# Kernel optimization log

Measured on AMD Instinct MI355X. Metric: run time of the kernel, lower is better.

The kernel has to match this reference:

```python
import jax, jax.numpy as jnp
import numpy as np

B, T, DIN, DOUT = 32, 3136, 192, 384
H, QS, WS = 6, 4, 16            # heads, q_stride, window_size (post-pool)
HD = DOUT // H                   # head_dim = 64
INNER = QS * WS                  # tokens per mask unit before pooling = 64
NW = T // INNER                  # num_windows = 49
MLP_HID = 4 * DOUT
EPS = 1e-5


def layer_norm(x, w, b):
    mu = x.mean(-1, keepdims=True)
    var = ((x - mu) ** 2).mean(-1, keepdims=True)
    return (x - mu) * jax.lax.rsqrt(var + EPS) * w + b


def setup_inputs() -> dict:
    key = jax.random.key(0)
    ks = jax.random.split(key, 16)
    rn = lambda k, shp, fan: jax.random.normal(k, shp, jnp.float32) * (fan ** -0.5)
    return {
        "embeddings": jax.random.normal(ks[0], (B, T, DIN), jnp.float32),
        "norm1_w": jnp.ones((DIN,), jnp.float32),
        "norm1_b": jnp.zeros((DIN,), jnp.float32),
        "w_qkv": rn(ks[1], (3 * DOUT, DIN), DIN),
        "b_qkv": jnp.zeros((3 * DOUT,), jnp.float32),
        "w_attn_proj": rn(ks[2], (DOUT, DOUT), DOUT),
        "b_attn_proj": jnp.zeros((DOUT,), jnp.float32),
        "w_res_proj": rn(ks[3], (DOUT, DIN), DIN),
        "b_res_proj": jnp.zeros((DOUT,), jnp.float32),
        "norm2_w": jnp.ones((DOUT,), jnp.float32),
        "norm2_b": jnp.zeros((DOUT,), jnp.float32),
        "w_fc1": rn(ks[4], (MLP_HID, DOUT), DOUT),
        "b_fc1": jnp.zeros((MLP_HID,), jnp.float32),
        "w_fc2": rn(ks[5], (DOUT, MLP_HID), MLP_HID),
        "b_fc2": jnp.zeros((DOUT,), jnp.float32),
    }


def _block(embeddings, norm1_w, norm1_b, w_qkv, b_qkv, w_attn_proj, b_attn_proj,
           w_res_proj, b_res_proj, norm2_w, norm2_b, w_fc1, b_fc1, w_fc2, b_fc2):
    x = layer_norm(embeddings, norm1_w, norm1_b)                 # [B,T,DIN]

    # residual path: project then do_pool (max over q_stride groups)
    res = x @ w_res_proj.T + b_res_proj                          # [B,T,DOUT]
    res = res.reshape(B, QS, T // QS, DOUT).max(axis=1)          # [B,T/QS,DOUT]

    # mask-unit attention
    qkv = x @ w_qkv.T + b_qkv                                    # [B,T,3*DOUT]
    qkv = qkv.reshape(B, INNER, NW, 3, H, HD)
    qkv = jnp.transpose(qkv, (3, 0, 4, 2, 1, 5))                 # [3,B,H,NW,INNER,HD]
    q, k, v = qkv[0], qkv[1], qkv[2]
    q = q.reshape(B, H, NW, QS, WS, HD).max(axis=3)              # q-pool -> [B,H,NW,WS,HD]
    scale = HD ** -0.5
    attn = jax.nn.softmax(jnp.einsum("bhwqd,bhwkd->bhwqk", q * scale, k), axis=-1)
    out = jnp.einsum("bhwqk,bhwkd->bhwqd", attn, v)              # [B,H,NW,WS,HD]
    out = jnp.transpose(out, (0, 3, 2, 1, 4)).reshape(B, WS * NW, DOUT)
    out = out @ w_attn_proj.T + b_attn_proj

    emb = res + out
    h = layer_norm(emb, norm2_w, norm2_b)
    h = jax.nn.gelu(h @ w_fc1.T + b_fc1, approximate=False)
    emb = emb + (h @ w_fc2.T + b_fc2)
    return emb, attn


def reference(embeddings, norm1_w, norm1_b, w_qkv, b_qkv, w_attn_proj, b_attn_proj,
              w_res_proj, b_res_proj, norm2_w, norm2_b, w_fc1, b_fc1, w_fc2, b_fc2):
    return _block(embeddings, norm1_w, norm1_b, w_qkv, b_qkv, w_attn_proj, b_attn_proj,
                  w_res_proj, b_res_proj, norm2_w, norm2_b, w_fc1, b_fc1, w_fc2, b_fc2)
```

## Files before the change

### kernel.cpp

```cpp
#include <hip/hip_runtime.h>
#include <stdint.h>

typedef __bf16 bf16_t;
typedef __attribute__((ext_vector_type(8))) __bf16 bf16x8;
typedef __attribute__((ext_vector_type(4))) __bf16 bf16x4;
typedef __attribute__((ext_vector_type(4))) float f32x4;

#define NB_ 32
#define NT_ 3136
#define DIN_ 192
#define DOUT_ 384
#define NH_ 6
#define HD_ 64
#define NW_ 49
#define WSZ_ 16
#define TP_ 784
#define MLP_ 1536

__device__ __forceinline__ f32x4 mfma16(bf16x8 a, bf16x8 b, f32x4 c) {
  return __builtin_amdgcn_mfma_f32_16x16x32_bf16(a, b, c, 0, 0, 0);
}

__device__ __forceinline__ void gload_lds16(const bf16_t* g, bf16_t* l) {
  __builtin_amdgcn_global_load_lds(
      (const __attribute__((address_space(1))) void*)((const void*)g),
      (__attribute__((address_space(3))) void*)l, 16, 0, 0);
}

__device__ __forceinline__ float gelu_tanh(float v) {
  const float t2 = 1.5957691216f * (v + 0.044715f * v * v * v);
  return v * (1.f - 1.f / (1.f + __expf(t2)));
}

__global__ void cvt_kernel(const float* __restrict__ s0, const float* __restrict__ s1,
                           const float* __restrict__ s2, const float* __restrict__ s3,
                           const float* __restrict__ s4, bf16_t* __restrict__ d0,
                           bf16_t* __restrict__ d1, bf16_t* __restrict__ d2,
                           bf16_t* __restrict__ d3, bf16_t* __restrict__ d4) {
  const int b = blockIdx.x;
  const float* s; bf16_t* d; long off;
  if (b < 108)      { s = s0; d = d0; off = (long)b * 2048; }
  else if (b < 144) { s = s1; d = d1; off = (long)(b - 108) * 2048; }
  else if (b < 216) { s = s2; d = d2; off = (long)(b - 144) * 2048; }
  else if (b < 504) { s = s3; d = d3; off = (long)(b - 216) * 2048; }
  else              { s = s4; d = d4; off = (long)(b - 504) * 2048; }
  off += (long)threadIdx.x * 8;
  const float4 a = *(const float4*)(s + off);
  const float4 c = *(const float4*)(s + off + 4);
  bf16x8 o;
  o[0] = (bf16_t)a.x; o[1] = (bf16_t)a.y; o[2] = (bf16_t)a.z; o[3] = (bf16_t)a.w;
  o[4] = (bf16_t)c.x; o[5] = (bf16_t)c.y; o[6] = (bf16_t)c.z; o[7] = (bf16_t)c.w;
  *(bf16x8*)(d + off) = o;
}

template <int D>
__global__ void ln_f32_kernel(const float* __restrict__ in, const float* __restrict__ w,
                              const float* __restrict__ bvec, bf16_t* __restrict__ out) {
  const int row = blockIdx.x * 4 + (threadIdx.x >> 6);
  const int lane = threadIdx.x & 63;
  constexpr int PER = D / 64;
  const float* x = in + (long)row * D;
  float v[PER];
  float s = 0.f;
#pragma unroll
  for (int i = 0; i < PER; i++) { v[i] = x[lane * PER + i]; s += v[i]; }
#pragma unroll
  for (int off = 1; off < 64; off <<= 1) s += __shfl_xor(s, off);
  const float mu = s * (1.f / D);
  float s2 = 0.f;
#pragma unroll
  for (int i = 0; i < PER; i++) { const float d = v[i] - mu; s2 += d * d; }
#pragma unroll
  for (int off = 1; off < 64; off <<= 1) s2 += __shfl_xor(s2, off);
  const float rstd = rsqrtf(s2 * (1.f / D) + 1e-5f);
  bf16_t* o = out + (long)row * D;
#pragma unroll
  for (int i = 0; i < PER; i++) {
    const int c = lane * PER + i;
    o[c] = (bf16_t)((v[i] - mu) * rstd * w[c] + bvec[c]);
  }
}

template <int D>
__global__ void ln_bf16_kernel(const bf16_t* __restrict__ in, const float* __restrict__ w,
                               const float* __restrict__ bvec, bf16_t* __restrict__ out) {
  const int row = blockIdx.x * 4 + (threadIdx.x >> 6);
  const int lane = threadIdx.x & 63;
  constexpr int PER = D / 64;
  const bf16_t* x = in + (long)row * D;
  float v[PER];
  float s = 0.f;
#pragma unroll
  for (int i = 0; i < PER; i++) { v[i] = (float)x[lane * PER + i]; s += v[i]; }
#pragma unroll
  for (int off = 1; off < 64; off <<= 1) s += __shfl_xor(s, off);
  const float mu = s * (1.f / D);
  float s2 = 0.f;
#pragma unroll
  for (int i = 0; i < PER; i++) { const float d = v[i] - mu; s2 += d * d; }
#pragma unroll
  for (int off = 1; off < 64; off <<= 1) s2 += __shfl_xor(s2, off);
  const float rstd = rsqrtf(s2 * (1.f / D) + 1e-5f);
  bf16_t* o = out + (long)row * D;
#pragma unroll
  for (int i = 0; i < PER; i++) {
    const int c = lane * PER + i;
    o[c] = (bf16_t)((v[i] - mu) * rstd * w[c] + bvec[c]);
  }
}

template <int ACT, int POOL>
__global__ __launch_bounds__(512, 4) void gemm8(
    const bf16_t* __restrict__ A, const bf16_t* __restrict__ W,
    const float* __restrict__ bias, bf16_t* __restrict__ C,
    int M, int N, int K) {
  __shared__ __align__(16) char AsB[256 * 128];
  __shared__ __align__(16) char WsB[128 * 128];

  const int nwg = gridDim.x;
  const int q = nwg >> 3, rm = nwg & 7;
  const int xcd = blockIdx.x & 7, idx = blockIdx.x >> 3;
  const int wg = (xcd < rm ? xcd * (q + 1) : rm * (q + 1) + (xcd - rm) * q) + idx;

  const int nbn = N >> 7;
  const int bmi = wg / nbn;
  const int bni = wg - bmi * nbn;
  const int m0 = bmi << 8, n0 = bni << 7;
  const int tid = threadIdx.x;
  const int lane = tid & 63;
  const int wid = tid >> 6;
  const int wr = (wid >> 1) * 64, wc = (wid & 1) * 64;
  const int l15 = lane & 15;
  const int lkb = (lane >> 4) << 4;
  const int srow = tid >> 3;
  const int scolsw = ((tid & 7) << 3) ^ ((srow & 7) << 3);
  const int swzr = (l15 & 7) << 4;

  f32x4 acc[4][4];
  const f32x4 zero = {0.f, 0.f, 0.f, 0.f};
#pragma unroll
  for (int i = 0; i < 4; i++)
#pragma unroll
    for (int j = 0; j < 4; j++) acc[i][j] = zero;

  long arow[4];
#pragma unroll
  for (int p = 0; p < 4; p++) {
    const int m = m0 + p * 64 + srow;
    if constexpr (POOL) {
      const int b = m / NT_;
      const int mm = m - b * NT_;
      arow[p] = (long)b * NT_ + (mm & 3) * TP_ + (mm >> 2);
    } else {
      arow[p] = m;
    }
  }
  long wrow[2];
#pragma unroll
  for (int p = 0; p < 2; p++) wrow[p] = (long)(n0 + p * 64 + srow);

  for (int k0 = 0; k0 < K; k0 += 64) {
    __syncthreads();
#pragma unroll
    for (int p = 0; p < 4; p++)
      gload_lds16(A + arow[p] * K + k0 + scolsw, (bf16_t*)(AsB + p * 8192 + tid * 16));
#pragma unroll
    for (int p = 0; p < 2; p++)
      gload_lds16(W + wrow[p] * K + k0 + scolsw, (bf16_t*)(WsB + p * 8192 + tid * 16));
    __syncthreads();
#pragma unroll
    for (int kk = 0; kk < 2; kk++) {
      bf16x8 af[4], wf[4];
#pragma unroll
      for (int i = 0; i < 4; i++)
        af[i] = *(const bf16x8*)(AsB + (wr + i * 16 + l15) * 128 + ((kk * 64 + lkb) ^ swzr));
#pragma unroll
      for (int j = 0; j < 4; j++)
        wf[j] = *(const bf16x8*)(WsB + (wc + j * 16 + l15) * 128 + ((kk * 64 + lkb) ^ swzr));
#pragma unroll
      for (int i = 0; i < 4; i++)
#pragma unroll
        for (int j = 0; j < 4; j++) {
          if constexpr (POOL) acc[i][j] = mfma16(af[i], wf[j], acc[i][j]);
          else                acc[i][j] = mfma16(wf[j], af[i], acc[i][j]);
        }
    }
  }

  const int rg = (lane >> 4) * 4;
  if constexpr (POOL) {
#pragma unroll
    for (int j = 0; j < 4; j++) {
      const int gn = n0 + wc + j * 16 + l15;
      const float bv = bias[gn];
#pragma unroll
      for (int i = 0; i < 4; i++) {
        const float v = fmaxf(fmaxf(acc[i][j][0], acc[i][j][1]),
                              fmaxf(acc[i][j][2], acc[i][j][3])) + bv;
        const long pm = (long)((m0 + wr + i * 16 + rg) >> 2);
        C[pm * N + gn] = (bf16_t)v;
      }
    }
  } else {
    __syncthreads();
    char* scr = AsB + wid * 4096;
#pragma unroll
    for (int i = 0; i < 4; i++) {
#pragma unroll
      for (int j = 0; j < 4; j++)
        *(f32x4*)(scr + l15 * 256 + ((((j * 16 + rg) << 2)) ^ ((l15 & 7) << 4))) = acc[i][j];
#pragma unroll
      for (int k = 0; k < 4; k++) {
        const int rl = k * 4 + (lane >> 4);
        const int cb = (lane & 15) << 4;
        const f32x4 v = *(const f32x4*)(scr + rl * 256 + (cb ^ ((rl & 7) << 4)));
        const long gm = m0 + wr + i * 16 + rl;
        const int gn = n0 + wc + ((lane & 15) << 2);
        const float4 bv = *(const float4*)(bias + gn);
        float vv[4] = {v[0] + bv.x, v[1] + bv.y, v[2] + bv.z, v[3] + bv.w};
        if constexpr (ACT == 1) {
#pragma unroll
          for (int r = 0; r < 4; r++) vv[r] = gelu_tanh(vv[r]);
        }
        bf16x4 o;
#pragma unroll
        for (int r = 0; r < 4; r++) o[r] = (bf16_t)vv[r];
        *(bf16x4*)(C + gm * N + gn) = o;
      }
    }
  }
}

template <int HASRES, int OF32, int RF32>
__global__ __launch_bounds__(256) void gemm_t(
    const bf16_t* __restrict__ A, const bf16_t* __restrict__ W,
    const float* __restrict__ bias, const void* __restrict__ resv,
    void* __restrict__ Cv, int M, int N, int K) {
  constexpr int BM = 64;
  constexpr int PA = BM / 32;
  constexpr int ABYTES = BM * 128;
  constexpr int BUFSZ = ABYTES + 128 * 128;
  __shared__ __align__(16) char LDSB[2 * BUFSZ];

  const int nwg = gridDim.x;
  const int q = nwg >> 3, rm = nwg & 7;
  const int xcd = blockIdx.x & 7, idx = blockIdx.x >> 3;
  const int wg = (xcd < rm ? xcd * (q + 1) : rm * (q + 1) + (xcd - rm) * q) + idx;

  const int nbn = N >> 7;
  const int bmi = wg / nbn;
  const int bni = wg - bmi * nbn;
  const int m0 = bmi * BM, n0 = bni << 7;
  const int tid = threadIdx.x;
  const int lane = tid & 63;
  const int wid = tid >> 6;
  const int wr = (wid >> 1) * 32, wc = (wid & 1) * 64;
  const int l15 = lane & 15;
  const int lkb = (lane >> 4) << 4;
  const int srow = tid >> 3;
  const int scolsw = ((tid & 7) << 3) ^ ((srow & 7) << 3);
  const int swzr = (l15 & 7) << 4;

  f32x4 acc[PA][4];
  const f32x4 zero = {0.f, 0.f, 0.f, 0.f};
#pragma unroll
  for (int i = 0; i < PA; i++)
#pragma unroll
    for (int j = 0; j < 4; j++) acc[i][j] = zero;

  long arow[PA];
#pragma unroll
  for (int p = 0; p < PA; p++) arow[p] = m0 + srow + p * 32;
  long wrow[4];
#pragma unroll
  for (int p = 0; p < 4; p++) wrow[p] = (long)(n0 + srow + p * 32);

  auto stage = [&](int buf, int k0) {
    char* base = LDSB + buf * BUFSZ;
#pragma unroll
    for (int p = 0; p < PA; p++)
      gload_lds16(A + arow[p] * K + k0 + scolsw, (bf16_t*)(base + p * 4096 + tid * 16));
#pragma unroll
    for (int p = 0; p < 4; p++)
      gload_lds16(W + wrow[p] * K + k0 + scolsw,
                  (bf16_t*)(base + ABYTES + p * 4096 + tid * 16));
  };

  const int nt = K >> 6;
  stage(0, 0);
  int cur = 0;
  for (int t = 0; t < nt; t++) {
    __syncthreads();
    if (t + 1 < nt) stage(cur ^ 1, (t + 1) << 6);
    const char* base = LDSB + cur * BUFSZ;
#pragma unroll
    for (int kk = 0; kk < 2; kk++) {
      bf16x8 af[PA], wf[4];
#pragma unroll
      for (int i = 0; i < PA; i++)
        af[i] = *(const bf16x8*)(base + (wr + i * 16 + l15) * 128 + ((kk * 64 + lkb) ^ swzr));
#pragma unroll
      for (int j = 0; j < 4; j++)
        wf[j] = *(const bf16x8*)(base + ABYTES + (wc + j * 16 + l15) * 128 +
                                 ((kk * 64 + lkb) ^ swzr));
#pragma unroll
      for (int i = 0; i < PA; i++)
#pragma unroll
        for (int j = 0; j < 4; j++) acc[i][j] = mfma16(wf[j], af[i], acc[i][j]);
    }
    cur ^= 1;
  }

  __syncthreads();
  char* scr = LDSB + wid * 8192;
  const int rg = (lane >> 4) * 4;
#pragma unroll
  for (int i = 0; i < PA; i++) {
    const int ml = i * 16 + l15;
#pragma unroll
    for (int j = 0; j < 4; j++)
      *(f32x4*)(scr + ml * 256 + ((((j * 16 + rg) << 2)) ^ ((ml & 7) << 4))) = acc[i][j];
  }
#pragma unroll
  for (int k = 0; k < 8; k++) {
    const int rl = k * 4 + (lane >> 4);
    const int cb = (lane & 15) << 4;
    const f32x4 v = *(const f32x4*)(scr + rl * 256 + (cb ^ ((rl & 7) << 4)));
    const long gm = m0 + wr + rl;
    const int gn = n0 + wc + ((lane & 15) << 2);
    const float4 bv = *(const float4*)(bias + gn);
    float vv[4] = {v[0] + bv.x, v[1] + bv.y, v[2] + bv.z, v[3] + bv.w};
    if constexpr (HASRES) {
      if constexpr (RF32) {
        const float4 rv = *(const float4*)((const float*)resv + gm * N + gn);
        vv[0] += rv.x; vv[1] += rv.y; vv[2] += rv.z; vv[3] += rv.w;
      } else {
        const bf16x4 rv = *(const bf16x4*)((const bf16_t*)resv + gm * N + gn);
#pragma unroll
        for (int r = 0; r < 4; r++) vv[r] += (float)rv[r];
      }
    }
    if constexpr (OF32) {
      float4 o = {vv[0], vv[1], vv[2], vv[3]};
      *(float4*)((float*)Cv + gm * N + gn) = o;
    } else {
      bf16x4 o;
#pragma unroll
      for (int r = 0; r < 4; r++) o[r] = (bf16_t)vv[r];
      *(bf16x4*)((bf16_t*)Cv + gm * N + gn) = o;
    }
  }
}

__global__ __launch_bounds__(384) void qkv_attn_kernel(
    const bf16_t* __restrict__ x, const bf16_t* __restrict__ Wqkv,
    const float* __restrict__ bq, float* __restrict__ prob,
    bf16_t* __restrict__ obuf) {
  __shared__ __align__(16) char As[64 * 384];
  __shared__ __align__(16) char Qs[6][2048];
  __shared__ __align__(16) char Kb[6][4096];
  const int b = blockIdx.x / NW_;
  const int w = blockIdx.x - b * NW_;
  const int tid = threadIdx.x;
  const int lane = tid & 63;
  const int h = tid >> 6;
  const int l15 = lane & 15;
  const int lk8 = (lane >> 4) * 8;
  const int lkb = (lane >> 4) << 4;
  const int rg = (lane >> 4) * 4;
  const f32x4 zero = {0.f, 0.f, 0.f, 0.f};

#pragma unroll
  for (int i = 0; i < 4; i++) {
    const int row = i * 16 + tid / 24;
    const int cb = ((tid % 24) * 16) ^ ((row & 7) << 4);
    gload_lds16(x + ((long)b * NT_ + (long)row * NW_ + w) * DIN_ + cb / 2,
                (bf16_t*)(As + i * 6144 + tid * 16));
  }
  __syncthreads();

  char* Qw = Qs[h];
  char* Bw = Kb[h];
  auto gemm_part = [&](int which, f32x4 (&acc)[4][4]) {
#pragma unroll
    for (int i = 0; i < 4; i++)
#pragma unroll
      for (int j = 0; j < 4; j++) acc[i][j] = zero;
#pragma unroll
    for (int j = 0; j < 4; j++) {
      const bf16_t* wrow = Wqkv + (long)(which * DOUT_ + h * HD_ + j * 16 + l15) * DIN_;
      bf16x8 wf[6];
#pragma unroll
      for (int ks = 0; ks < 6; ks++)
        wf[ks] = *(const bf16x8*)(wrow + ks * 32 + lk8);
#pragma unroll
      for (int ks = 0; ks < 6; ks++) {
#pragma unroll
        for (int i = 0; i < 4; i++) {
          const int mr = i * 16 + l15;
          const bf16x8 af = *(const bf16x8*)(As + mr * 384 +
                                             ((ks * 64 + lkb) ^ ((mr & 7) << 4)));
          acc[i][j] = mfma16(af, wf[ks], acc[i][j]);
        }
      }
    }
  };

  f32x4 acc[4][4];
  gemm_part(0, acc);
#pragma unroll
  for (int j = 0; j < 4; j++) {
    const float bb = bq[h * HD_ + j * 16 + l15];
#pragma unroll
    for (int r = 0; r < 4; r++) {
      const float v = (fmaxf(fmaxf(acc[0][j][r], acc[1][j][r]),
                             fmaxf(acc[2][j][r], acc[3][j][r])) + bb) * 0.125f;
      const int row = rg + r;
      *(bf16_t*)(Qw + row * 128 + (((j * 16 + l15) * 2) ^ ((row & 7) << 4))) = (bf16_t)v;
    }
  }
  bf16x8 aq[2];
#pragma unroll
  for (int kc = 0; kc < 2; kc++)
    aq[kc] = *(const bf16x8*)(Qw + l15 * 128 + ((kc * 64 + lkb) ^ ((l15 & 7) << 4)));

  gemm_part(1, acc);
#pragma unroll
  for (int j = 0; j < 4; j++) {
    const float bb = bq[DOUT_ + h * HD_ + j * 16 + l15];
#pragma unroll
    for (int i = 0; i < 4; i++)
#pragma unroll
      for (int r = 0; r < 4; r++) acc[i][j][r] += bb;
  }
  f32x4 s4[4];
#pragma unroll
  for (int nc = 0; nc < 4; nc++) s4[nc] = zero;
#pragma unroll
  for (int t = 0; t < 2; t++) {
#pragma unroll
    for (int i2 = 0; i2 < 2; i2++) {
      const int i = t * 2 + i2;
#pragma unroll
      for (int j = 0; j < 4; j++)
#pragma unroll
        for (int r = 0; r < 4; r++) {
          const int tokh = i2 * 16 + rg + r;
          *(bf16_t*)(Bw + tokh * 128 + (((j * 16 + l15) * 2) ^ ((tokh & 7) << 4))) =
              (bf16_t)acc[i][j][r];
        }
    }
#pragma unroll
    for (int nch = 0; nch < 2; nch++) {
      const int nc = t * 2 + nch;
      const int tokh = nch * 16 + l15;
#pragma unroll
      for (int kc = 0; kc < 2; kc++) {
        const bf16x8 bk = *(const bf16x8*)(Bw + tokh * 128 +
                                           ((kc * 64 + lkb) ^ ((tokh & 7) << 4)));
        s4[nc] = mfma16(aq[kc], bk, s4[nc]);
      }
    }
  }

#pragma unroll
  for (int r = 0; r < 4; r++) {
    float mx = fmaxf(fmaxf(s4[0][r], s4[1][r]), fmaxf(s4[2][r], s4[3][r]));
#pragma unroll
    for (int off = 1; off < 16; off <<= 1) mx = fmaxf(mx, __shfl_xor(mx, off));
    float sm = 0.f;
#pragma unroll
    for (int nc = 0; nc < 4; nc++) {
      const float p = __expf(s4[nc][r] - mx);
      s4[nc][r] = p;
      sm += p;
    }
#pragma unroll
    for (int off = 1; off < 16; off <<= 1) sm += __shfl_xor(sm, off);
    const float inv = 1.f / sm;
#pragma unroll
    for (int nc = 0; nc < 4; nc++) s4[nc][r] *= inv;
  }

  float* aout = prob + (long)((b * NH_ + h) * NW_ + w) * (WSZ_ * 64);
#pragma unroll
  for (int nc = 0; nc < 4; nc++) {
#pragma unroll
    for (int r = 0; r < 4; r++) {
      const int row = rg + r, col = nc * 16 + l15;
      aout[row * 64 + col] = s4[nc][r];
      *(bf16_t*)(Qw + row * 128 + ((col * 2) ^ ((row & 7) << 4))) = (bf16_t)s4[nc][r];
    }
  }
  bf16x8 ap[2];
#pragma unroll
  for (int kc = 0; kc < 2; kc++)
    ap[kc] = *(const bf16x8*)(Qw + l15 * 128 + ((kc * 64 + lkb) ^ ((l15 & 7) << 4)));

  gemm_part(2, acc);
#pragma unroll
  for (int j = 0; j < 4; j++) {
    const float bb = bq[2 * DOUT_ + h * HD_ + j * 16 + l15];
#pragma unroll
    for (int i = 0; i < 4; i++)
#pragma unroll
      for (int r = 0; r < 4; r++) acc[i][j][r] += bb;
  }
  f32x4 o4[4];
#pragma unroll
  for (int nc = 0; nc < 4; nc++) o4[nc] = zero;
#pragma unroll
  for (int t = 0; t < 2; t++) {
#pragma unroll
    for (int i2 = 0; i2 < 2; i2++) {
      const int i = t * 2 + i2;
#pragma unroll
      for (int j = 0; j < 4; j++)
#pragma unroll
        for (int r = 0; r < 4; r++) {
          const int tokh = i2 * 16 + rg + r;
          *(bf16_t*)(Bw + tokh * 128 + (((j * 16 + l15) * 2) ^ ((tokh & 7) << 4))) =
              (bf16_t)acc[i][j][r];
        }
    }
#pragma unroll
    for (int nc = 0; nc < 4; nc++) {
      bf16x8 bv;
#pragma unroll
      for (int e = 0; e < 8; e++) {
        const int tokh = lk8 + e;
        bv[e] = *(const bf16_t*)(Bw + tokh * 128 +
                                 (((nc * 16 + l15) * 2) ^ ((tokh & 7) << 4)));
      }
      o4[nc] = mfma16(ap[t], bv, o4[nc]);
    }
  }

  bf16_t* ob = obuf + (long)b * TP_ * DOUT_;
#pragma unroll
  for (int nc = 0; nc < 4; nc++) {
#pragma unroll
    for (int r = 0; r < 4; r++) {
      const int wsr = rg + r;
      const int tprime = wsr * NW_ + w;
      const int chan = h * HD_ + nc * 16 + l15;
      ob[(long)tprime * DOUT_ + chan] = (bf16_t)o4[nc][r];
    }
  }
}

extern "C" void kernel_launch(void* const* d_in, const int* in_sizes, int n_in,
                              void* d_out, int out_size, void* d_ws, size_t ws_size,
                              hipStream_t stream) {
  const float* emb   = (const float*)d_in[0];
  const float* n1w   = (const float*)d_in[1];
  const float* n1b   = (const float*)d_in[2];
  const float* wqkv  = (const float*)d_in[3];
  const float* bqkv  = (const float*)d_in[4];
  const float* wproj = (const float*)d_in[5];
  const float* bproj = (const float*)d_in[6];
  const float* wres  = (const float*)d_in[7];
  const float* bres  = (const float*)d_in[8];
  const float* n2w   = (const float*)d_in[9];
  const float* n2b   = (const float*)d_in[10];
  const float* wfc1  = (const float*)d_in[11];
  const float* bfc1  = (const float*)d_in[12];
  const float* wfc2  = (const float*)d_in[13];
  const float* bfc2  = (const float*)d_in[14];
  float* out = (float*)d_out;

  const int BT = NB_ * NT_;
  const int BTP = NB_ * TP_;

  char* wsb = (char*)d_ws;
  bf16_t* x    = (bf16_t*)(wsb);
  bf16_t* h1   = (bf16_t*)(wsb);
  bf16_t* obuf = (bf16_t*)(wsb + 57802752L);
  bf16_t* resp = (bf16_t*)(wsb + 77070336L);
  bf16_t* h0   = resp;
  bf16_t* emb1 = (bf16_t*)(wsb + 96337920L);
  bf16_t* wbqkv = (bf16_t*)(wsb + 115605504L);
  bf16_t* wbres = wbqkv + 221184L;
  bf16_t* wbproj = wbres + 73728L;
  bf16_t* wbfc1 = wbproj + 147456L;
  bf16_t* wbfc2 = wbfc1 + 589824L;
  float*  prob = out + 9633792L;

  cvt_kernel<<<792, 256, 0, stream>>>(wqkv, wres, wproj, wfc1, wfc2,
                                      wbqkv, wbres, wbproj, wbfc1, wbfc2);
  ln_f32_kernel<DIN_><<<BT / 4, 256, 0, stream>>>(emb, n1w, n1b, x);
  gemm8<0, 1><<<(BT / 256) * (DOUT_ / 128), 512, 0, stream>>>(
      x, wbres, bres, resp, BT, DOUT_, DIN_);
  qkv_attn_kernel<<<NB_ * NW_, 384, 0, stream>>>(x, wbqkv, bqkv, prob, obuf);
  gemm_t<1, 0, 0><<<(BTP / 64) * (DOUT_ / 128), 256, 0, stream>>>(
      obuf, wbproj, bproj, resp, emb1, BTP, DOUT_, DOUT_);
  ln_bf16_kernel<DOUT_><<<BTP / 4, 256, 0, stream>>>(emb1, n2w, n2b, h0);
  gemm8<1, 0><<<(BTP / 256) * (MLP_ / 128), 512, 0, stream>>>(
      h0, wbfc1, bfc1, h1, BTP, MLP_, DOUT_);
  gemm_t<1, 1, 0><<<(BTP / 64) * (DOUT_ / 128), 256, 0, stream>>>(
      h1, wbfc2, bfc2, emb1, out, BTP, DOUT_, MLP_);
}
```

Baseline: 312.8 us.

## Stream QKV GEMM per column block with double-buffered weight prefetch

Restructures the fused QKV+attention kernel so each 16-column block of the Q/K/V projection is computed with only four accumulators and written straight to LDS, instead of holding a full 64x64 accumulator tile in registers. Weight fragments for the next block are prefetched into a second register buffer while the current block runs MFMAs. K and V tiles are now stored whole in a larger per-wave LDS region, which replaces the separate Q buffer, and the XOR swizzle changes. This lowers register pressure and hides global weight-load latency, at the cost of more LDS per block, which could reduce occupancy.

```diff
diff --git a/kernel.cpp b/kernel.cpp
--- a/kernel.cpp
+++ b/kernel.cpp
@@ -357,8 +357,7 @@
     const float* __restrict__ bq, float* __restrict__ prob,
     bf16_t* __restrict__ obuf) {
   __shared__ __align__(16) char As[64 * 384];
-  __shared__ __align__(16) char Qs[6][2048];
-  __shared__ __align__(16) char Kb[6][4096];
+  __shared__ __align__(16) char Kb[6][8192];
   const int b = blockIdx.x / NW_;
   const int w = blockIdx.x - b * NW_;
   const int tid = threadIdx.x;
@@ -369,6 +368,7 @@
   const int lkb = (lane >> 4) << 4;
   const int rg = (lane >> 4) * 4;
   const f32x4 zero = {0.f, 0.f, 0.f, 0.f};
+  char* Bw = Kb[h];
 
 #pragma unroll
   for (int i = 0; i < 4; i++) {
@@ -379,87 +379,89 @@
   }
   __syncthreads();
 
-  char* Qw = Qs[h];
-  char* Bw = Kb[h];
-  auto gemm_part = [&](int which, f32x4 (&acc)[4][4]) {
+  auto loadW = [&](int which, int j, bf16x8* wf) {
+    const bf16_t* wrow = Wqkv + (long)(which * DOUT_ + h * HD_ + j * 16 + l15) * DIN_;
+#pragma unroll
+    for (int ks = 0; ks < 6; ks++) wf[ks] = *(const bf16x8*)(wrow + ks * 32 + lk8);
+  };
+  auto bwb = [&](int row, int colb) {
+    return row * 128 + (colb ^ (((row >> 2) & 3) << 5));
+  };
+
+  bf16x8 wfA[6], wfB[6];
+  loadW(0, 0, wfA);
+
+#pragma unroll
+  for (int j = 0; j < 4; j++) {
+    bf16x8* cur = (j & 1) ? wfB : wfA;
+    bf16x8* nxt = (j & 1) ? wfA : wfB;
+    if (j < 3) loadW(0, j + 1, nxt);
+    else       loadW(1, 0, nxt);
+    f32x4 a4[4];
+#pragma unroll
+    for (int i = 0; i < 4; i++) a4[i] = zero;
+#pragma unroll
+    for (int ks = 0; ks < 6; ks++) {
+#pragma unroll
+      for (int i = 0; i < 4; i++) {
+        const int mr = i * 16 + l15;
+        const bf16x8 af = *(const bf16x8*)(As + mr * 384 +
+                                           ((ks * 64 + lkb) ^ ((mr & 7) << 4)));
+        a4[i] = mfma16(af, cur[ks], a4[i]);
+      }
+    }
+    const float bb = bq[h * HD_ + j * 16 + l15];
+#pragma unroll
+    for (int r = 0; r < 4; r++) {
+      const float v = (fmaxf(fmaxf(a4[0][r], a4[1][r]),
+                             fmaxf(a4[2][r], a4[3][r])) + bb) * 0.125f;
+      const int row = rg + r;
+      *(bf16_t*)(Bw + bwb(row, (j * 16 + l15) * 2)) = (bf16_t)v;
+    }
+  }
+  bf16x8 aq[2];
+#pragma unroll
+  for (int kc = 0; kc < 2; kc++)
+    aq[kc] = *(const bf16x8*)(Bw + bwb(l15, kc * 64 + lkb));
+
+#pragma unroll
+  for (int j = 0; j < 4; j++) {
+    bf16x8* cur = (j & 1) ? wfB : wfA;
+    bf16x8* nxt = (j & 1) ? wfA : wfB;
+    if (j < 3) loadW(1, j + 1, nxt);
+    else       loadW(2, 0, nxt);
+    f32x4 a4[4];
+#pragma unroll
+    for (int i = 0; i < 4; i++) a4[i] = zero;
+#pragma unroll
+    for (int ks = 0; ks < 6; ks++) {
+#pragma unroll
+      for (int i = 0; i < 4; i++) {
+        const int mr = i * 16 + l15;
+        const bf16x8 af = *(const bf16x8*)(As + mr * 384 +
+                                           ((ks * 64 + lkb) ^ ((mr & 7) << 4)));
+        a4[i] = mfma16(af, cur[ks], a4[i]);
+      }
+    }
+    const float bb = bq[DOUT_ + h * HD_ + j * 16 + l15];
 #pragma unroll
     for (int i = 0; i < 4; i++)
 #pragma unroll
-      for (int j = 0; j < 4; j++) acc[i][j] = zero;
-#pragma unroll
-    for (int j = 0; j < 4; j++) {
-      const bf16_t* wrow = Wqkv + (long)(which * DOUT_ + h * HD_ + j * 16 + l15) * DIN_;
-      bf16x8 wf[6];
-#pragma unroll
-      for (int ks = 0; ks < 6; ks++)
-        wf[ks] = *(const bf16x8*)(wrow + ks * 32 + lk8);
-#pragma unroll
-      for (int ks = 0; ks < 6; ks++) {
-#pragma unroll
-        for (int i = 0; i < 4; i++) {
-          const int mr = i * 16 + l15;
-          const bf16x8 af = *(const bf16x8*)(As + mr * 384 +
-                                             ((ks * 64 + lkb) ^ ((mr & 7) << 4)));
-          acc[i][j] = mfma16(af, wf[ks], acc[i][j]);
-        }
-      }
-    }
-  };
-
-  f32x4 acc[4][4];
-  gemm_part(0, acc);
-#pragma unroll
-  for (int j = 0; j < 4; j++) {
-    const float bb = bq[h * HD_ + j * 16 + l15];
-#pragma unroll
-    for (int r = 0; r < 4; r++) {
-      const float v = (fmaxf(fmaxf(acc[0][j][r], acc[1][j][r]),
-                             fmaxf(acc[2][j][r], acc[3][j][r])) + bb) * 0.125f;
-      const int row = rg + r;
-      *(bf16_t*)(Qw + row * 128 + (((j * 16 + l15) * 2) ^ ((row & 7) << 4))) = (bf16_t)v;
-    }
-  }
-  bf16x8 aq[2];
-#pragma unroll
-  for (int kc = 0; kc < 2; kc++)
-    aq[kc] = *(const bf16x8*)(Qw + l15 * 128 + ((kc * 64 + lkb) ^ ((l15 & 7) << 4)));
-
-  gemm_part(1, acc);
-#pragma unroll
-  for (int j = 0; j < 4; j++) {
-    const float bb = bq[DOUT_ + h * HD_ + j * 16 + l15];
-#pragma unroll
-    for (int i = 0; i < 4; i++)
-#pragma unroll
-      for (int r = 0; r < 4; r++) acc[i][j][r] += bb;
-  }
+      for (int r = 0; r < 4; r++) {
+        const int row = i * 16 + rg + r;
+        *(bf16_t*)(Bw + bwb(row, (j * 16 + l15) * 2)) = (bf16_t)(a4[i][r] + bb);
+      }
+  }
+
   f32x4 s4[4];
 #pragma unroll
   for (int nc = 0; nc < 4; nc++) s4[nc] = zero;
 #pragma unroll
-  for (int t = 0; t < 2; t++) {
-#pragma unroll
-    for (int i2 = 0; i2 < 2; i2++) {
-      const int i = t * 2 + i2;
-#pragma unroll
-      for (int j = 0; j < 4; j++)
-#pragma unroll
-        for (int r = 0; r < 4; r++) {
-          const int tokh = i2 * 16 + rg + r;
-          *(bf16_t*)(Bw + tokh * 128 + (((j * 16 + l15) * 2) ^ ((tokh & 7) << 4))) =
-              (bf16_t)acc[i][j][r];
-        }
-    }
-#pragma unroll
-    for (int nch = 0; nch < 2; nch++) {
-      const int nc = t * 2 + nch;
-      const int tokh = nch * 16 + l15;
-#pragma unroll
-      for (int kc = 0; kc < 2; kc++) {
-        const bf16x8 bk = *(const bf16x8*)(Bw + tokh * 128 +
-                                           ((kc * 64 + lkb) ^ ((tokh & 7) << 4)));
-        s4[nc] = mfma16(aq[kc], bk, s4[nc]);
-      }
+  for (int nc = 0; nc < 4; nc++) {
+#pragma unroll
+    for (int kc = 0; kc < 2; kc++) {
+      const bf16x8 bk = *(const bf16x8*)(Bw + bwb(nc * 16 + l15, kc * 64 + lkb));
+      s4[nc] = mfma16(aq[kc], bk, s4[nc]);
     }
   }
 
@@ -489,50 +491,56 @@
     for (int r = 0; r < 4; r++) {
       const int row = rg + r, col = nc * 16 + l15;
       aout[row * 64 + col] = s4[nc][r];
-      *(bf16_t*)(Qw + row * 128 + ((col * 2) ^ ((row & 7) << 4))) = (bf16_t)s4[nc][r];
+      *(bf16_t*)(Bw + bwb(row, col * 2)) = (bf16_t)s4[nc][r];
     }
   }
   bf16x8 ap[2];
 #pragma unroll
   for (int kc = 0; kc < 2; kc++)
-    ap[kc] = *(const bf16x8*)(Qw + l15 * 128 + ((kc * 64 + lkb) ^ ((l15 & 7) << 4)));
-
-  gemm_part(2, acc);
+    ap[kc] = *(const bf16x8*)(Bw + bwb(l15, kc * 64 + lkb));
+
 #pragma unroll
   for (int j = 0; j < 4; j++) {
+    bf16x8* cur = (j & 1) ? wfB : wfA;
+    bf16x8* nxt = (j & 1) ? wfA : wfB;
+    if (j < 3) loadW(2, j + 1, nxt);
+    f32x4 a4[4];
+#pragma unroll
+    for (int i = 0; i < 4; i++) a4[i] = zero;
+#pragma unroll
+    for (int ks = 0; ks < 6; ks++) {
+#pragma unroll
+      for (int i = 0; i < 4; i++) {
+        const int mr = i * 16 + l15;
+        const bf16x8 af = *(const bf16x8*)(As + mr * 384 +
+                                           ((ks * 64 + lkb) ^ ((mr & 7) << 4)));
+        a4[i] = mfma16(af, cur[ks], a4[i]);
+      }
+    }
     const float bb = bq[2 * DOUT_ + h * HD_ + j * 16 + l15];
 #pragma unroll
     for (int i = 0; i < 4; i++)
 #pragma unroll
-      for (int r = 0; r < 4; r++) acc[i][j][r] += bb;
-  }
+      for (int r = 0; r < 4; r++) {
+        const int row = i * 16 + rg + r;
+        *(bf16_t*)(Bw + bwb(row, (j * 16 + l15) * 2)) = (bf16_t)(a4[i][r] + bb);
+      }
+  }
+
   f32x4 o4[4];
 #pragma unroll
   for (int nc = 0; nc < 4; nc++) o4[nc] = zero;
 #pragma unroll
-  for (int t = 0; t < 2; t++) {
-#pragma unroll
-    for (int i2 = 0; i2 < 2; i2++) {
-      const int i = t * 2 + i2;
-#pragma unroll
-      for (int j = 0; j < 4; j++)
-#pragma unroll
-        for (int r = 0; r < 4; r++) {
-          const int tokh = i2 * 16 + rg + r;
-          *(bf16_t*)(Bw + tokh * 128 + (((j * 16 + l15) * 2) ^ ((tokh & 7) << 4))) =
-              (bf16_t)acc[i][j][r];
-        }
-    }
+  for (int kc = 0; kc < 2; kc++) {
 #pragma unroll
     for (int nc = 0; nc < 4; nc++) {
       bf16x8 bv;
 #pragma unroll
       for (int e = 0; e < 8; e++) {
-        const int tokh = lk8 + e;
-        bv[e] = *(const bf16_t*)(Bw + tokh * 128 +
-                                 (((nc * 16 + l15) * 2) ^ ((tokh & 7) << 4)));
-      }
-      o4[nc] = mfma16(ap[t], bv, o4[nc]);
+        const int tok = kc * 32 + lk8 + e;
+        bv[e] = *(const bf16_t*)(Bw + bwb(tok, (nc * 16 + l15) * 2));
+      }
+      o4[nc] = mfma16(ap[kc], bv, o4[nc]);
     }
   }
 
```

Result: slower. 331.4 us (+5.9%).
